# Kernel optimization log

Hardware: AMD Instinct MI355X
Metric: run time of the kernel (lower is better)

## Reference

```python
import jax, jax.numpy as jnp
import numpy as np

N_NODES = 50000
N_EDGES = 800000
D_FEAT = 96
PROMPT_DIM = 96


def setup_inputs() -> dict:
    key = jax.random.key(0)
    k1, k2, k3, k4 = jax.random.split(key, 4)
    graph_embedding = jax.random.normal(k1, (N_NODES, D_FEAT), dtype=jnp.float32)
    weight = jax.random.normal(k2, (1, PROMPT_DIM), dtype=jnp.float32)
    src = jax.random.randint(k3, (N_EDGES,), 0, N_NODES, dtype=jnp.int64)
    dst = jax.random.randint(k4, (N_EDGES,), 0, N_NODES, dtype=jnp.int64)
    return {"graph_embedding": graph_embedding, "weight": weight,
            "src": src, "dst": dst, "num_nodes": N_NODES}


def reference(graph_embedding, weight, src, dst, num_nodes):
    # message on edge e: concat(ft[src[e]], weight)  -> [E, D_FEAT + PROMPT_DIM]
    # reduce: sum of messages over incoming edges of each dst node.
    # Feature half: scatter-sum of gathered src features.
    agg_ft = jax.ops.segment_sum(graph_embedding[src], dst, num_segments=num_nodes)
    # Prompt half: identical prompt on every edge => in_degree[v] * weight.
    ones = jnp.ones((src.shape[0],), dtype=graph_embedding.dtype)
    in_deg = jax.ops.segment_sum(ones, dst, num_segments=num_nodes)  # [N]
    agg_p = in_deg[:, None] * weight  # [N, PROMPT_DIM] (weight broadcasts from [1,P])
    return jnp.concatenate([agg_ft, agg_p], axis=1)
```

## Files before the change

### kernel.cpp

```cpp
#include <hip/hip_runtime.h>

#define D_FEAT 96
#define P_DIM 96
#define OUT_DIM 192
#define SCAN_BLK 256
#define NODES_PER_BLK 8
#define LPN 24
#define RNG_SHIFT 8
#define RNG_NODES 256
#define NBLK_A 256
#define BIG_T 1024
#define FS_CAP 6144

#define HAVE_FP8 1

typedef float f32x4 __attribute__((ext_vector_type(4)));
typedef float f32x2 __attribute__((ext_vector_type(2)));
typedef unsigned int u32;
typedef u32 u32x4 __attribute__((ext_vector_type(4)));
typedef u32 u32x2 __attribute__((ext_vector_type(2)));

__global__ __launch_bounds__(256) void zero_k(float* __restrict__ out,
                                              float* __restrict__ deg,
                                              int n_out, int n_deg) {
    int stride = gridDim.x * blockDim.x;
    for (int i = blockIdx.x * blockDim.x + threadIdx.x; i < n_out; i += stride)
        out[i] = 0.0f;
    for (int i = blockIdx.x * blockDim.x + threadIdx.x; i < n_deg; i += stride)
        deg[i] = 0.0f;
}

__global__ __launch_bounds__(256) void degf_k(const int* __restrict__ dst,
                                              float* __restrict__ deg,
                                              int n_edges) {
    int e = blockIdx.x * blockDim.x + threadIdx.x;
    if (e < n_edges) atomicAdd(deg + dst[e], 1.0f);
}

__global__ __launch_bounds__(256) void scatter_k(const float* __restrict__ emb,
                                                 const int* __restrict__ src,
                                                 const int* __restrict__ dst,
                                                 float* __restrict__ out,
                                                 int n_edges) {
    int idx = blockIdx.x * blockDim.x + threadIdx.x;
    int e = idx / D_FEAT;
    if (e >= n_edges) return;
    int c = idx - e * D_FEAT;
    atomicAdd(out + (size_t)dst[e] * OUT_DIM + c, emb[(size_t)src[e] * D_FEAT + c]);
}

__global__ __launch_bounds__(256) void prompt_k(const float* __restrict__ w,
                                                const float* __restrict__ deg,
                                                float* __restrict__ out,
                                                int n_nodes) {
    int idx = blockIdx.x * blockDim.x + threadIdx.x;
    if (idx >= n_nodes * P_DIM) return;
    int v = idx / P_DIM;
    int c = idx - v * P_DIM;
    out[(size_t)v * OUT_DIM + P_DIM + c] = deg[v] * w[c];
}


__device__ __forceinline__ u32 f2bf_rn(float f) {
    u32 b = __float_as_uint(f);
    return (b + 0x7fffu + ((b >> 16) & 1u)) >> 16;
}

#if HAVE_FP8
__device__ __forceinline__ u32 enc4_fp8(float a, float b, float c, float d) {
    u32 r = __builtin_amdgcn_cvt_pk_fp8_f32(a, b, 0u, false);
    r = __builtin_amdgcn_cvt_pk_fp8_f32(c, d, r, true);
    return r;
}
#endif


__global__ __launch_bounds__(BIG_T) void conv_hist_k(
        const f32x4* __restrict__ emb4, u32x4* __restrict__ embq,
        int nq, int mode,
        const int* __restrict__ dst, int* __restrict__ cnt,
        int n_edges, int nr, int chunk) {
    int b = blockIdx.x, t = threadIdx.x;
    int gs = gridDim.x * BIG_T;
    int gid = b * BIG_T + t;
    if (mode == 1) {
        for (int i = gid; i < nq; i += gs) {
            f32x4 a = emb4[2 * i];
            f32x4 c = emb4[2 * i + 1];
            u32x4 o;
            o.x = f2bf_rn(a.x) | (f2bf_rn(a.y) << 16);
            o.y = f2bf_rn(a.z) | (f2bf_rn(a.w) << 16);
            o.z = f2bf_rn(c.x) | (f2bf_rn(c.y) << 16);
            o.w = f2bf_rn(c.z) | (f2bf_rn(c.w) << 16);
            embq[i] = o;
        }
    }
#if HAVE_FP8
    else if (mode == 2) {
        for (int i = gid; i < nq; i += gs) {
            f32x4 a = emb4[4 * i];
            f32x4 b4 = emb4[4 * i + 1];
            f32x4 c = emb4[4 * i + 2];
            f32x4 d = emb4[4 * i + 3];
            u32x4 o;
            o.x = enc4_fp8(a.x, a.y, a.z, a.w);
            o.y = enc4_fp8(b4.x, b4.y, b4.z, b4.w);
            o.z = enc4_fp8(c.x, c.y, c.z, c.w);
            o.w = enc4_fp8(d.x, d.y, d.z, d.w);
            embq[i] = o;
        }
    }
#endif
    __shared__ int h[RNG_NODES];
    if (t < RNG_NODES) h[t] = 0;
    __syncthreads();
    int beg = b * chunk;
    int end = beg + chunk; if (end > n_edges) end = n_edges;
    for (int i = beg + t; i < end; i += BIG_T)
        atomicAdd(&h[dst[i] >> RNG_SHIFT], 1);
    __syncthreads();
    if (t < nr) cnt[t * NBLK_A + b] = h[t];
}

__global__ __launch_bounds__(SCAN_BLK) void scan_block_k(int* __restrict__ cnt,
                                                         int* __restrict__ aux, int n) {
    __shared__ int buf[SCAN_BLK];
    int t = threadIdx.x;
    int i = blockIdx.x * SCAN_BLK + t;
    int v = (i < n) ? cnt[i] : 0;
    buf[t] = v;
    __syncthreads();
    for (int off = 1; off < SCAN_BLK; off <<= 1) {
        int x = (t >= off) ? buf[t - off] : 0;
        __syncthreads();
        buf[t] += x;
        __syncthreads();
    }
    if (i < n) cnt[i] = buf[t] - v;
    if (t == SCAN_BLK - 1) aux[blockIdx.x] = buf[t];
}

__global__ __launch_bounds__(BIG_T) void binwrite_k(const int* __restrict__ src,
                                                    const int* __restrict__ dst,
                                                    const int* __restrict__ cnt,
                                                    const int* __restrict__ aux,
                                                    int* __restrict__ pack,
                                                    int n_edges, int nr, int chunk) {
    __shared__ int buf[SCAN_BLK];
    __shared__ int cur[RNG_NODES];
    int b = blockIdx.x, t = threadIdx.x;
    int av = 0;
    if (t < SCAN_BLK) { av = (t < nr) ? aux[t] : 0; buf[t] = av; }
    __syncthreads();
    for (int off = 1; off < SCAN_BLK; off <<= 1) {
        int x = 0;
        if (t < SCAN_BLK && t >= off) x = buf[t - off];
        __syncthreads();
        if (t < SCAN_BLK) buf[t] += x;
        __syncthreads();
    }
    if (t < nr) cur[t] = (buf[t] - av) + cnt[t * NBLK_A + b];
    __syncthreads();
    int beg = b * chunk;
    int end = beg + chunk; if (end > n_edges) end = n_edges;
    for (int i = beg + t; i < end; i += BIG_T) {
        int d = dst[i];
        int pos = atomicAdd(&cur[d >> RNG_SHIFT], 1);
        pack[pos] = (src[i] << RNG_SHIFT) | (d & (RNG_NODES - 1));
    }
}

__global__ __launch_bounds__(BIG_T) void finesort_k(const int* __restrict__ aux,
                                                    const int* __restrict__ pack,
                                                    int* __restrict__ offs,
                                                    int* __restrict__ sorted_src,
                                                    int n_nodes, int n_edges, int nr) {
    __shared__ int buf[SCAN_BLK];
    __shared__ int h[RNG_NODES];
    __shared__ int cur[RNG_NODES];
    __shared__ int win[FS_CAP];
    int r = blockIdx.x, t = threadIdx.x;
    int av = 0;
    if (t < SCAN_BLK) { av = (t < nr) ? aux[t] : 0; buf[t] = av; }
    __syncthreads();
    for (int off = 1; off < SCAN_BLK; off <<= 1) {
        int x = 0;
        if (t < SCAN_BLK && t >= off) x = buf[t - off];
        __syncthreads();
        if (t < SCAN_BLK) buf[t] += x;
        __syncthreads();
    }
    int start = buf[r] - aux[r];
    int end = buf[r];
    int wlen = end - start;
    bool fits = (wlen <= FS_CAP);
    if (t < RNG_NODES) h[t] = 0;
    __syncthreads();
    if (fits) {
        for (int i = t; i < wlen; i += BIG_T) {
            int p = pack[start + i];
            win[i] = p;
            atomicAdd(&h[p & (RNG_NODES - 1)], 1);
        }
    } else {
        for (int i = start + t; i < end; i += BIG_T)
            atomicAdd(&h[pack[i] & (RNG_NODES - 1)], 1);
    }
    __syncthreads();
    int v = (t < RNG_NODES) ? h[t] : 0;
    for (int off = 1; off < RNG_NODES; off <<= 1) {
        int x = 0;
        if (t < RNG_NODES && t >= off) x = h[t - off];
        __syncthreads();
        if (t < RNG_NODES) h[t] += x;
        __syncthreads();
    }
    if (t < RNG_NODES) {
        int o = start + h[t] - v;
        int node = (r << RNG_SHIFT) + t;
        if (node < n_nodes) offs[node] = o;
        cur[t] = o;
    }
    __syncthreads();
    if (fits) {
        for (int i = t; i < wlen; i += BIG_T) {
            int p = win[i];
            int pos = atomicAdd(&cur[p & (RNG_NODES - 1)], 1);
            sorted_src[pos] = p >> RNG_SHIFT;
        }
    } else {
        for (int i = start + t; i < end; i += BIG_T) {
            int p = pack[i];
            int pos = atomicAdd(&cur[p & (RNG_NODES - 1)], 1);
            sorted_src[pos] = p >> RNG_SHIFT;
        }
    }
}


#if HAVE_FP8
#define DEC8(A, g)                                                          \
    {                                                                       \
        A[0] += __builtin_amdgcn_cvt_pk_f32_fp8((g).x, false);              \
        A[1] += __builtin_amdgcn_cvt_pk_f32_fp8((g).x, true);               \
        A[2] += __builtin_amdgcn_cvt_pk_f32_fp8((g).y, false);              \
        A[3] += __builtin_amdgcn_cvt_pk_f32_fp8((g).y, true);               \
    }

__global__ __launch_bounds__(192) void aggf8_k(
        const u32x2* __restrict__ emb8,
        const float* __restrict__ w,
        const int* __restrict__ offs,
        const int* __restrict__ sorted_src,
        float* __restrict__ out, int n_nodes, int n_edges) {
    int t = threadIdx.x;
    int sub = t / 12;
    int lane = t - sub * 12;
    int node = blockIdx.x * 16 + sub;
    if (node >= n_nodes) return;

    int start = offs[node];
    int endp = (node + 1 < n_nodes) ? offs[node + 1] : n_edges;
    int cnt = endp - start;
    const int* sp = sorted_src + start;

    f32x2 A[4], B[4];
    #pragma unroll
    for (int k = 0; k < 4; ++k) { A[k] = (f32x2){0.f, 0.f}; B[k] = (f32x2){0.f, 0.f}; }

    int j = 0;
    if (cnt >= 8) {
        int s0 = sp[0], s1 = sp[1], s2 = sp[2], s3 = sp[3];
        for (; j + 7 < cnt; j += 4) {
            int t0 = sp[j + 4], t1 = sp[j + 5], t2 = sp[j + 6], t3 = sp[j + 7];
            u32x2 g0 = emb8[(size_t)s0 * 12 + lane];
            u32x2 g1 = emb8[(size_t)s1 * 12 + lane];
            u32x2 g2 = emb8[(size_t)s2 * 12 + lane];
            u32x2 g3 = emb8[(size_t)s3 * 12 + lane];
            DEC8(A, g0); DEC8(B, g1); DEC8(A, g2); DEC8(B, g3);
            s0 = t0; s1 = t1; s2 = t2; s3 = t3;
        }
        u32x2 g0 = emb8[(size_t)s0 * 12 + lane];
        u32x2 g1 = emb8[(size_t)s1 * 12 + lane];
        u32x2 g2 = emb8[(size_t)s2 * 12 + lane];
        u32x2 g3 = emb8[(size_t)s3 * 12 + lane];
        DEC8(A, g0); DEC8(B, g1); DEC8(A, g2); DEC8(B, g3);
        j += 4;
    }
    for (; j + 3 < cnt; j += 4) {
        int s0 = sp[j], s1 = sp[j + 1], s2 = sp[j + 2], s3 = sp[j + 3];
        u32x2 g0 = emb8[(size_t)s0 * 12 + lane];
        u32x2 g1 = emb8[(size_t)s1 * 12 + lane];
        u32x2 g2 = emb8[(size_t)s2 * 12 + lane];
        u32x2 g3 = emb8[(size_t)s3 * 12 + lane];
        DEC8(A, g0); DEC8(B, g1); DEC8(A, g2); DEC8(B, g3);
    }
    for (; j < cnt; ++j) {
        u32x2 g0 = emb8[(size_t)sp[j] * 12 + lane];
        DEC8(A, g0);
    }

    f32x4 lo = {A[0].x + B[0].x, A[0].y + B[0].y, A[1].x + B[1].x, A[1].y + B[1].y};
    f32x4 hi = {A[2].x + B[2].x, A[2].y + B[2].y, A[3].x + B[3].x, A[3].y + B[3].y};

    f32x4* outrow = (f32x4*)(out + (size_t)node * OUT_DIM);
    const f32x4* w4 = (const f32x4*)w;
    float c = (float)cnt;
    f32x4 plo = c * w4[lane * 2];
    f32x4 phi = c * w4[lane * 2 + 1];
    __builtin_nontemporal_store(lo, outrow + lane * 2);
    __builtin_nontemporal_store(hi, outrow + lane * 2 + 1);
    __builtin_nontemporal_store(plo, outrow + 24 + lane * 2);
    __builtin_nontemporal_store(phi, outrow + 24 + lane * 2 + 1);
}
#endif


#define ACC8(A, g)                                                        \
    {                                                                     \
        A[0] += __uint_as_float((g).x << 16);                             \
        A[1] += __uint_as_float((g).x & 0xffff0000u);                     \
        A[2] += __uint_as_float((g).y << 16);                             \
        A[3] += __uint_as_float((g).y & 0xffff0000u);                     \
        A[4] += __uint_as_float((g).z << 16);                             \
        A[5] += __uint_as_float((g).z & 0xffff0000u);                     \
        A[6] += __uint_as_float((g).w << 16);                             \
        A[7] += __uint_as_float((g).w & 0xffff0000u);                     \
    }

__global__ __launch_bounds__(192) void aggb_k(
        const u32x4* __restrict__ embb,
        const float* __restrict__ w,
        const int* __restrict__ offs,
        const int* __restrict__ sorted_src,
        float* __restrict__ out, int n_nodes, int n_edges) {
    int t = threadIdx.x;
    int sub = t / 12;
    int lane = t - sub * 12;
    int node = blockIdx.x * 16 + sub;
    if (node >= n_nodes) return;

    int start = offs[node];
    int endp = (node + 1 < n_nodes) ? offs[node + 1] : n_edges;
    int cnt = endp - start;
    const int* sp = sorted_src + start;

    float aA[8] = {0.f, 0.f, 0.f, 0.f, 0.f, 0.f, 0.f, 0.f};
    float aB[8] = {0.f, 0.f, 0.f, 0.f, 0.f, 0.f, 0.f, 0.f};
    int j = 0;
    if (cnt >= 8) {
        int s0 = sp[0], s1 = sp[1], s2 = sp[2], s3 = sp[3];
        for (; j + 7 < cnt; j += 4) {
            int t0 = sp[j + 4], t1 = sp[j + 5], t2 = sp[j + 6], t3 = sp[j + 7];
            u32x4 g0 = embb[(size_t)s0 * 12 + lane];
            u32x4 g1 = embb[(size_t)s1 * 12 + lane];
            u32x4 g2 = embb[(size_t)s2 * 12 + lane];
            u32x4 g3 = embb[(size_t)s3 * 12 + lane];
            ACC8(aA, g0); ACC8(aB, g1); ACC8(aA, g2); ACC8(aB, g3);
            s0 = t0; s1 = t1; s2 = t2; s3 = t3;
        }
        u32x4 g0 = embb[(size_t)s0 * 12 + lane];
        u32x4 g1 = embb[(size_t)s1 * 12 + lane];
        u32x4 g2 = embb[(size_t)s2 * 12 + lane];
        u32x4 g3 = embb[(size_t)s3 * 12 + lane];
        ACC8(aA, g0); ACC8(aB, g1); ACC8(aA, g2); ACC8(aB, g3);
        j += 4;
    }
    for (; j + 3 < cnt; j += 4) {
        int s0 = sp[j], s1 = sp[j + 1], s2 = sp[j + 2], s3 = sp[j + 3];
        u32x4 g0 = embb[(size_t)s0 * 12 + lane];
        u32x4 g1 = embb[(size_t)s1 * 12 + lane];
        u32x4 g2 = embb[(size_t)s2 * 12 + lane];
        u32x4 g3 = embb[(size_t)s3 * 12 + lane];
        ACC8(aA, g0); ACC8(aB, g1); ACC8(aA, g2); ACC8(aB, g3);
    }
    for (; j < cnt; ++j) {
        u32x4 g0 = embb[(size_t)sp[j] * 12 + lane];
        ACC8(aA, g0);
    }

    f32x4 lo = {aA[0] + aB[0], aA[1] + aB[1], aA[2] + aB[2], aA[3] + aB[3]};
    f32x4 hi = {aA[4] + aB[4], aA[5] + aB[5], aA[6] + aB[6], aA[7] + aB[7]};

    f32x4* outrow = (f32x4*)(out + (size_t)node * OUT_DIM);
    const f32x4* w4 = (const f32x4*)w;
    float c = (float)cnt;
    f32x4 plo = c * w4[lane * 2];
    f32x4 phi = c * w4[lane * 2 + 1];
    __builtin_nontemporal_store(lo, outrow + lane * 2);
    __builtin_nontemporal_store(hi, outrow + lane * 2 + 1);
    __builtin_nontemporal_store(plo, outrow + 24 + lane * 2);
    __builtin_nontemporal_store(phi, outrow + 24 + lane * 2 + 1);
}

__global__ __launch_bounds__(NODES_PER_BLK * LPN) void agg4p_k(
        const f32x4* __restrict__ emb4,
        const f32x4* __restrict__ w4,
        const int* __restrict__ offs,
        const int* __restrict__ sorted_src,
        float* __restrict__ out, int n_nodes, int n_edges) {
    int t = threadIdx.x;
    int sub = t / LPN;
    int lane = t - sub * LPN;
    int node = blockIdx.x * NODES_PER_BLK + sub;
    if (node >= n_nodes) return;

    int start = offs[node];
    int endp = (node + 1 < n_nodes) ? offs[node + 1] : n_edges;
    int cnt = endp - start;
    const int* sp = sorted_src + start;

    f32x4 a0 = {0.f, 0.f, 0.f, 0.f};
    f32x4 a1 = a0, a2 = a0, a3 = a0;
    int j = 0;
    for (; j + 3 < cnt; j += 4) {
        int s0 = sp[j], s1 = sp[j + 1], s2 = sp[j + 2], s3 = sp[j + 3];
        f32x4 v0 = emb4[(size_t)s0 * LPN + lane];
        f32x4 v1 = emb4[(size_t)s1 * LPN + lane];
        f32x4 v2 = emb4[(size_t)s2 * LPN + lane];
        f32x4 v3 = emb4[(size_t)s3 * LPN + lane];
        a0 += v0; a1 += v1; a2 += v2; a3 += v3;
    }
    for (; j < cnt; ++j) {
        a0 += emb4[(size_t)sp[j] * LPN + lane];
    }
    f32x4 ft = (a0 + a1) + (a2 + a3);

    f32x4* outrow = (f32x4*)(out + (size_t)node * OUT_DIM);
    float c = (float)cnt;
    f32x4 pv = c * w4[lane];
    __builtin_nontemporal_store(ft, outrow + lane);
    __builtin_nontemporal_store(pv, outrow + LPN + lane);
}

extern "C" void kernel_launch(void* const* d_in, const int* in_sizes, int n_in,
                              void* d_out, int out_size, void* d_ws, size_t ws_size,
                              hipStream_t stream) {
    const float* emb = (const float*)d_in[0];
    const float* w   = (const float*)d_in[1];
    const int*   src = (const int*)d_in[2];
    const int*   dst = (const int*)d_in[3];
    float* out = (float*)d_out;

    const int n_nodes = in_sizes[0] / D_FEAT;
    const int n_edges = in_sizes[2];
    const int nr = (n_nodes + RNG_NODES - 1) >> RNG_SHIFT;
    const int cnt_len = nr * NBLK_A;
    const int nb_cnt = (cnt_len + SCAN_BLK - 1) / SCAN_BLK;
    const int chunk = (n_edges + NBLK_A - 1) / NBLK_A;

    size_t base_ints = (size_t)cnt_len + SCAN_BLK + n_nodes + 2 * (size_t)n_edges;
    size_t embq_off  = (base_ints + 3) & ~(size_t)3;
    size_t need_f32  = base_ints * sizeof(int);
    size_t need_bf16 = (embq_off + (size_t)n_nodes * 48) * sizeof(int);
    size_t need_fp8  = (embq_off + (size_t)n_nodes * 24) * sizeof(int);
    bool ok = (nr <= SCAN_BLK) && (nb_cnt <= SCAN_BLK) &&
              (n_nodes <= (1 << (31 - RNG_SHIFT - 1)));

    if (ws_size < need_f32 || !ok) {
        float* deg = (float*)d_ws;
        int n_out = n_nodes * OUT_DIM;
        int blocks = (n_out + 255) / 256;
        if (blocks > 2048) blocks = 2048;
        zero_k<<<blocks, 256, 0, stream>>>(out, deg, n_out, n_nodes);
        degf_k<<<(n_edges + 255) / 256, 256, 0, stream>>>(dst, deg, n_edges);
        long long total = (long long)n_edges * D_FEAT;
        scatter_k<<<(int)((total + 255) / 256), 256, 0, stream>>>(emb, src, dst, out, n_edges);
        prompt_k<<<(n_nodes * P_DIM + 255) / 256, 256, 0, stream>>>(w, deg, out, n_nodes);
        return;
    }

    int* cnt        = (int*)d_ws;
    int* aux        = cnt + cnt_len;
    int* offs       = aux + SCAN_BLK;
    int* pack       = offs + n_nodes;
    int* sorted_src = pack + n_edges;
    u32x4* embq     = (u32x4*)((int*)d_ws + embq_off);

    int mode = 0;
    int nq = 0;
#if HAVE_FP8
    if (ws_size >= need_fp8) { mode = 2; nq = n_nodes * 6; }
    else if (ws_size >= need_bf16) { mode = 1; nq = n_nodes * 12; }
#else
    if (ws_size >= need_bf16) { mode = 1; nq = n_nodes * 12; }
#endif

    conv_hist_k<<<NBLK_A, BIG_T, 0, stream>>>((const f32x4*)emb, embq, nq, mode,
                                              dst, cnt, n_edges, nr, chunk);
    scan_block_k<<<nb_cnt, SCAN_BLK, 0, stream>>>(cnt, aux, cnt_len);
    binwrite_k<<<NBLK_A, BIG_T, 0, stream>>>(src, dst, cnt, aux, pack, n_edges, nr, chunk);
    finesort_k<<<nr, BIG_T, 0, stream>>>(aux, pack, offs, sorted_src, n_nodes, n_edges, nr);
#if HAVE_FP8
    if (mode == 2) {
        aggf8_k<<<(n_nodes + 15) / 16, 192, 0, stream>>>(
            (const u32x2*)embq, w, offs, sorted_src, out, n_nodes, n_edges);
    } else
#endif
    if (mode == 1) {
        aggb_k<<<(n_nodes + 15) / 16, 192, 0, stream>>>(
            embq, w, offs, sorted_src, out, n_nodes, n_edges);
    } else {
        agg4p_k<<<(n_nodes + NODES_PER_BLK - 1) / NODES_PER_BLK, NODES_PER_BLK * LPN, 0, stream>>>(
            (const f32x4*)emb, (const f32x4*)w, offs, sorted_src, out, n_nodes, n_edges);
    }
}
```

Baseline: 53.16 us.

## Split FP8 embedding table into column halves and aggregate in two passes

The FP8-quantized embedding table is now stored as two separate half-tables (first 48 and last 48 features per node), and aggregation runs as two launches, each gathering only 48 bytes per source node into its half of the output columns. The goal is to shrink each pass's gather working set so the half-table fits better in cache (about 2.4 MB instead of 4.8 MB) and random gathers hit more often. In exchange, the CSR offsets and sorted source indices are read twice, there is an extra kernel launch, and each gather fetches a narrower 48-byte row segment.

```diff
diff --git a/kernel.cpp b/kernel.cpp
--- a/kernel.cpp
+++ b/kernel.cpp
@@ -76,7 +76,8 @@
 
 
 __global__ __launch_bounds__(BIG_T) void conv_hist_k(
-        const f32x4* __restrict__ emb4, u32x4* __restrict__ embq,
+        const f32x4* __restrict__ emb4,
+        u32x4* __restrict__ emblo, u32x4* __restrict__ embhi,
         int nq, int mode,
         const int* __restrict__ dst, int* __restrict__ cnt,
         int n_edges, int nr, int chunk) {
@@ -92,22 +93,23 @@
             o.y = f2bf_rn(a.z) | (f2bf_rn(a.w) << 16);
             o.z = f2bf_rn(c.x) | (f2bf_rn(c.y) << 16);
             o.w = f2bf_rn(c.z) | (f2bf_rn(c.w) << 16);
-            embq[i] = o;
+            emblo[i] = o;
         }
     }
 #if HAVE_FP8
     else if (mode == 2) {
         for (int i = gid; i < nq; i += gs) {
-            f32x4 a = emb4[4 * i];
-            f32x4 b4 = emb4[4 * i + 1];
-            f32x4 c = emb4[4 * i + 2];
-            f32x4 d = emb4[4 * i + 3];
+            int node = i / 6;
+            int g = i - node * 6;
+            const f32x4* srcp = emb4 + (size_t)node * 24 + g * 4;
+            f32x4 a = srcp[0], b4 = srcp[1], c = srcp[2], d = srcp[3];
             u32x4 o;
             o.x = enc4_fp8(a.x, a.y, a.z, a.w);
             o.y = enc4_fp8(b4.x, b4.y, b4.z, b4.w);
             o.z = enc4_fp8(c.x, c.y, c.z, c.w);
             o.w = enc4_fp8(d.x, d.y, d.z, d.w);
-            embq[i] = o;
+            if (g < 3) emblo[(size_t)node * 3 + g] = o;
+            else       embhi[(size_t)node * 3 + (g - 3)] = o;
         }
     }
 #endif
@@ -247,16 +249,17 @@
         A[3] += __builtin_amdgcn_cvt_pk_f32_fp8((g).y, true);               \
     }
 
-__global__ __launch_bounds__(192) void aggf8_k(
-        const u32x2* __restrict__ emb8,
+__global__ __launch_bounds__(192) void aggf8h_k(
+        const u32x2* __restrict__ table,
         const float* __restrict__ w,
         const int* __restrict__ offs,
         const int* __restrict__ sorted_src,
-        float* __restrict__ out, int n_nodes, int n_edges) {
+        float* __restrict__ out, int n_nodes, int n_edges,
+        int colbase4, int write_prompt) {
     int t = threadIdx.x;
-    int sub = t / 12;
-    int lane = t - sub * 12;
-    int node = blockIdx.x * 16 + sub;
+    int sub = t / 6;
+    int lane = t - sub * 6;
+    int node = blockIdx.x * 32 + sub;
     if (node >= n_nodes) return;
 
     int start = offs[node];
@@ -273,30 +276,30 @@
         int s0 = sp[0], s1 = sp[1], s2 = sp[2], s3 = sp[3];
         for (; j + 7 < cnt; j += 4) {
             int t0 = sp[j + 4], t1 = sp[j + 5], t2 = sp[j + 6], t3 = sp[j + 7];
-            u32x2 g0 = emb8[(size_t)s0 * 12 + lane];
-            u32x2 g1 = emb8[(size_t)s1 * 12 + lane];
-            u32x2 g2 = emb8[(size_t)s2 * 12 + lane];
-            u32x2 g3 = emb8[(size_t)s3 * 12 + lane];
+            u32x2 g0 = table[(size_t)s0 * 6 + lane];
+            u32x2 g1 = table[(size_t)s1 * 6 + lane];
+            u32x2 g2 = table[(size_t)s2 * 6 + lane];
+            u32x2 g3 = table[(size_t)s3 * 6 + lane];
             DEC8(A, g0); DEC8(B, g1); DEC8(A, g2); DEC8(B, g3);
             s0 = t0; s1 = t1; s2 = t2; s3 = t3;
         }
-        u32x2 g0 = emb8[(size_t)s0 * 12 + lane];
-        u32x2 g1 = emb8[(size_t)s1 * 12 + lane];
-        u32x2 g2 = emb8[(size_t)s2 * 12 + lane];
-        u32x2 g3 = emb8[(size_t)s3 * 12 + lane];
+        u32x2 g0 = table[(size_t)s0 * 6 + lane];
+        u32x2 g1 = table[(size_t)s1 * 6 + lane];
+        u32x2 g2 = table[(size_t)s2 * 6 + lane];
+        u32x2 g3 = table[(size_t)s3 * 6 + lane];
         DEC8(A, g0); DEC8(B, g1); DEC8(A, g2); DEC8(B, g3);
         j += 4;
     }
     for (; j + 3 < cnt; j += 4) {
         int s0 = sp[j], s1 = sp[j + 1], s2 = sp[j + 2], s3 = sp[j + 3];
-        u32x2 g0 = emb8[(size_t)s0 * 12 + lane];
-        u32x2 g1 = emb8[(size_t)s1 * 12 + lane];
-        u32x2 g2 = emb8[(size_t)s2 * 12 + lane];
-        u32x2 g3 = emb8[(size_t)s3 * 12 + lane];
+        u32x2 g0 = table[(size_t)s0 * 6 + lane];
+        u32x2 g1 = table[(size_t)s1 * 6 + lane];
+        u32x2 g2 = table[(size_t)s2 * 6 + lane];
+        u32x2 g3 = table[(size_t)s3 * 6 + lane];
         DEC8(A, g0); DEC8(B, g1); DEC8(A, g2); DEC8(B, g3);
     }
     for (; j < cnt; ++j) {
-        u32x2 g0 = emb8[(size_t)sp[j] * 12 + lane];
+        u32x2 g0 = table[(size_t)sp[j] * 6 + lane];
         DEC8(A, g0);
     }
 
@@ -304,14 +307,17 @@
     f32x4 hi = {A[2].x + B[2].x, A[2].y + B[2].y, A[3].x + B[3].x, A[3].y + B[3].y};
 
     f32x4* outrow = (f32x4*)(out + (size_t)node * OUT_DIM);
-    const f32x4* w4 = (const f32x4*)w;
-    float c = (float)cnt;
-    f32x4 plo = c * w4[lane * 2];
-    f32x4 phi = c * w4[lane * 2 + 1];
-    __builtin_nontemporal_store(lo, outrow + lane * 2);
-    __builtin_nontemporal_store(hi, outrow + lane * 2 + 1);
-    __builtin_nontemporal_store(plo, outrow + 24 + lane * 2);
-    __builtin_nontemporal_store(phi, outrow + 24 + lane * 2 + 1);
+    __builtin_nontemporal_store(lo, outrow + colbase4 + lane * 2);
+    __builtin_nontemporal_store(hi, outrow + colbase4 + lane * 2 + 1);
+    if (write_prompt) {
+        const f32x4* w4 = (const f32x4*)w;
+        float c = (float)cnt;
+        #pragma unroll
+        for (int k = 0; k < 4; ++k) {
+            f32x4 p = c * w4[lane * 4 + k];
+            __builtin_nontemporal_store(p, outrow + 24 + lane * 4 + k);
+        }
+    }
 }
 #endif
 
@@ -475,7 +481,8 @@
     int* offs       = aux + SCAN_BLK;
     int* pack       = offs + n_nodes;
     int* sorted_src = pack + n_edges;
-    u32x4* embq     = (u32x4*)((int*)d_ws + embq_off);
+    u32x4* emblo    = (u32x4*)((int*)d_ws + embq_off);
+    u32x4* embhi    = (u32x4*)((int*)d_ws + embq_off + (size_t)n_nodes * 12);
 
     int mode = 0;
     int nq = 0;
@@ -486,20 +493,26 @@
     if (ws_size >= need_bf16) { mode = 1; nq = n_nodes * 12; }
 #endif
 
-    conv_hist_k<<<NBLK_A, BIG_T, 0, stream>>>((const f32x4*)emb, embq, nq, mode,
-                                              dst, cnt, n_edges, nr, chunk);
+    conv_hist_k<<<NBLK_A, BIG_T, 0, stream>>>((const f32x4*)emb, emblo, embhi,
+                                              nq, mode, dst, cnt,
+                                              n_edges, nr, chunk);
     scan_block_k<<<nb_cnt, SCAN_BLK, 0, stream>>>(cnt, aux, cnt_len);
     binwrite_k<<<NBLK_A, BIG_T, 0, stream>>>(src, dst, cnt, aux, pack, n_edges, nr, chunk);
     finesort_k<<<nr, BIG_T, 0, stream>>>(aux, pack, offs, sorted_src, n_nodes, n_edges, nr);
 #if HAVE_FP8
     if (mode == 2) {
-        aggf8_k<<<(n_nodes + 15) / 16, 192, 0, stream>>>(
-            (const u32x2*)embq, w, offs, sorted_src, out, n_nodes, n_edges);
+        int blocks = (n_nodes + 31) / 32;
+        aggf8h_k<<<blocks, 192, 0, stream>>>((const u32x2*)emblo, w, offs,
+                                             sorted_src, out, n_nodes, n_edges,
+                                             0, 0);
+        aggf8h_k<<<blocks, 192, 0, stream>>>((const u32x2*)embhi, w, offs,
+                                             sorted_src, out, n_nodes, n_edges,
+                                             12, 1);
     } else
 #endif
     if (mode == 1) {
         aggb_k<<<(n_nodes + 15) / 16, 192, 0, stream>>>(
-            embq, w, offs, sorted_src, out, n_nodes, n_edges);
+            emblo, w, offs, sorted_src, out, n_nodes, n_edges);
     } else {
         agg4p_k<<<(n_nodes + NODES_PER_BLK - 1) / NODES_PER_BLK, NODES_PER_BLK * LPN, 0, stream>>>(
             (const f32x4*)emb, (const f32x4*)w, offs, sorted_src, out, n_nodes, n_edges);
```

After: 74.86 us. +40.8%, slower.
